# Optimization experiments

Measured on AMD Instinct MI355X. Metric: run time of the kernel, lower is better.

## Reference

```python
import jax, jax.numpy as jnp
import numpy as np

NEG_INF = -1e9


def setup_inputs() -> dict:
    key = jax.random.key(0)
    k1, k2, k3, k4 = jax.random.split(key, 4)
    B, H, M, N, D = 8, 16, 1024, 1024, 64
    return {
        "query": jax.random.normal(k1, (B, H, M, D), dtype=jnp.float32),
        "key": jax.random.normal(k2, (B, H, N, D), dtype=jnp.float32),
        "value": jax.random.normal(k3, (B, H, N, D), dtype=jnp.float32),
        "mask": jax.random.randint(k4, (B, H, N), 0, 2, dtype=jnp.int32),
    }


def reference(query, key, value, mask):
    # NOTE: faithful to source bug: scale uses key.size(-1) AFTER transpose,
    # i.e. N (sequence length), not d_h.
    N = key.shape[-2]
    scale = 1.0 / jnp.sqrt(jnp.asarray(N, dtype=query.dtype))
    # scores: [B, H, M, N]
    scores = jnp.einsum("bhmd,bhnd->bhmn", query, key) * scale
    scores = jnp.where(mask[:, :, None, :] == 0, jnp.asarray(NEG_INF, scores.dtype), scores)
    p_attn = jax.nn.softmax(scores, axis=-1)
    out = jnp.einsum("bhmn,bhnd->bhmd", p_attn, value)
    return out, p_attn
```

## Files before the change

kernel.cpp:

```cpp
#include <hip/hip_runtime.h>
#include <hip/hip_bf16.h>

#define BH 128
#define SEQ 1024
#define DH 64
#define MT 16
#define NW 256
#define PSTRIDE 1032

typedef __attribute__((ext_vector_type(8))) short short8;
typedef __attribute__((ext_vector_type(4))) float float4v;

__device__ __forceinline__ short bf16_rne(float x) {
    unsigned u = __builtin_bit_cast(unsigned, x);
    unsigned r = (u + 0x7fffu + ((u >> 16) & 1u)) >> 16;
    return (short)r;
}

__device__ __forceinline__ void bf16_split(float x, short& hi, short& lo) {
    unsigned u = __builtin_bit_cast(unsigned, x);
    hi = (short)(u >> 16);
    float hf = __builtin_bit_cast(float, u & 0xffff0000u);
    float res = x - hf;
    unsigned v = __builtin_bit_cast(unsigned, res);
    lo = (short)((v + 0x7fffu + ((v >> 16) & 1u)) >> 16);
}

__global__ __launch_bounds__(256, 4)
void attn_convert_kernel(const float* __restrict__ K, const float* __restrict__ V,
                         short* __restrict__ Khi, short* __restrict__ Klo,
                         short* __restrict__ Vt)
{
    const unsigned c = blockIdx.x * 256u + threadIdx.x;
    if (blockIdx.x < 4096) {
        const int bh = c >> 13;
        const int o8 = c & 8191;
        const int q  = o8 & 3;
        const int l  = (o8 >> 2) & 15;
        const int s  = (o8 >> 6) & 1;
        const int kb = o8 >> 7;
        const float* src = K + ((size_t)bh * SEQ + kb * 16 + l) * DH + s * 32 + q * 8;
        float4v x0 = *(const float4v*)src;
        float4v x1 = *(const float4v*)(src + 4);
        short8 hi, lo;
        #pragma unroll
        for (int j = 0; j < 4; ++j) {
            short h, w;
            bf16_split(x0[j], h, w); hi[j] = h;     lo[j] = w;
            bf16_split(x1[j], h, w); hi[4 + j] = h; lo[4 + j] = w;
        }
        *(short8*)(Khi + (size_t)c * 8) = hi;
        *(short8*)(Klo + (size_t)c * 8) = lo;
    } else {
        const unsigned c2 = c - 4096u * 256u;
        const int bh = c2 >> 13;
        const int o8 = c2 & 8191;
        const int lv = o8 & 15;
        const int k8 = (o8 >> 4) & 127;
        const int d4 = o8 >> 11;
        const float* src = V + ((size_t)bh * SEQ + k8 * 8) * DH + d4 * 16 + lv;
        short8 vv;
        #pragma unroll
        for (int j = 0; j < 8; ++j) vv[j] = bf16_rne(src[(size_t)j * DH]);
        *(short8*)(Vt + (size_t)c2 * 8) = vv;
    }
}

__global__ __launch_bounds__(256, 3)
void Attention_66889820668421_kernel(const float* __restrict__ Q,
                                     const short* __restrict__ Khi,
                                     const short* __restrict__ Klo,
                                     const short* __restrict__ Vt,
                                     const int*   __restrict__ mask,
                                     float* __restrict__ out,
                                     float* __restrict__ pattn)
{
    __shared__ short P_lds[MT * PSTRIDE];
    __shared__ float out_red[4][MT][DH];
    __shared__ float red_max[4][MT];
    __shared__ float red_sum[4][MT];

    const int tid  = threadIdx.x;
    const int wave = tid >> 6;
    const int lane = tid & 63;
    const int q    = lane >> 4;
    const int l    = lane & 15;
    const int bh   = blockIdx.y;
    const int m0   = blockIdx.x * MT;
    const int nbase = wave * NW;

    short8 a_hi[2], a_lo[2];
    {
        const float* qrow = Q + (size_t)(bh * SEQ + m0 + l) * DH;
        #pragma unroll
        for (int s = 0; s < 2; ++s) {
            float4v x0 = *(const float4v*)(qrow + s * 32 + q * 8);
            float4v x1 = *(const float4v*)(qrow + s * 32 + q * 8 + 4);
            #pragma unroll
            for (int j = 0; j < 4; ++j) {
                short h, lo2;
                bf16_split(x0[j], h, lo2); a_hi[s][j] = h; a_lo[s][j] = lo2;
                bf16_split(x1[j], h, lo2); a_hi[s][4 + j] = h; a_lo[s][4 + j] = lo2;
            }
        }
    }

    const short* khb = Khi + ((size_t)bh << 16);
    const short* klb = Klo + ((size_t)bh << 16);
    const short* vtb = Vt  + ((size_t)bh << 16);

    float4v acc[16];
    int mv[16];
    #pragma unroll
    for (int t = 0; t < 16; ++t) {
        const int kb   = (nbase >> 4) + t;
        const int off0 = kb * 1024 + l * 32 + q * 8;
        short8 b0h = *(const short8*)(khb + off0);
        short8 b0l = *(const short8*)(klb + off0);
        short8 b1h = *(const short8*)(khb + off0 + 512);
        short8 b1l = *(const short8*)(klb + off0 + 512);
        float4v a = {0.f, 0.f, 0.f, 0.f};
        a = __builtin_amdgcn_mfma_f32_16x16x32_bf16(a_hi[0], b0h, a, 0, 0, 0);
        a = __builtin_amdgcn_mfma_f32_16x16x32_bf16(a_hi[0], b0l, a, 0, 0, 0);
        a = __builtin_amdgcn_mfma_f32_16x16x32_bf16(a_lo[0], b0h, a, 0, 0, 0);
        a = __builtin_amdgcn_mfma_f32_16x16x32_bf16(a_hi[1], b1h, a, 0, 0, 0);
        a = __builtin_amdgcn_mfma_f32_16x16x32_bf16(a_hi[1], b1l, a, 0, 0, 0);
        a = __builtin_amdgcn_mfma_f32_16x16x32_bf16(a_lo[1], b1h, a, 0, 0, 0);
        mv[t] = mask[bh * SEQ + nbase + t * 16 + l];
        acc[t] = a;
    }

    const float scale = 0.03125f;
    float pm[4] = {-3e38f, -3e38f, -3e38f, -3e38f};
    #pragma unroll
    for (int t = 0; t < 16; ++t) {
        const bool ok = (mv[t] != 0);
        #pragma unroll
        for (int r = 0; r < 4; ++r) {
            float s = ok ? acc[t][r] * scale : -1e9f;
            acc[t][r] = s;
            pm[r] = fmaxf(pm[r], s);
        }
    }
    #pragma unroll
    for (int off = 1; off < 16; off <<= 1) {
        #pragma unroll
        for (int r = 0; r < 4; ++r)
            pm[r] = fmaxf(pm[r], __shfl_xor(pm[r], off));
    }
    if (l == 0) {
        #pragma unroll
        for (int r = 0; r < 4; ++r) red_max[wave][q * 4 + r] = pm[r];
    }
    __syncthreads();

    float rm[4];
    #pragma unroll
    for (int r = 0; r < 4; ++r) {
        const int row = q * 4 + r;
        rm[r] = fmaxf(fmaxf(red_max[0][row], red_max[1][row]),
                      fmaxf(red_max[2][row], red_max[3][row]));
    }

    float ps[4] = {0.f, 0.f, 0.f, 0.f};
    #pragma unroll
    for (int t = 0; t < 16; ++t) {
        #pragma unroll
        for (int r = 0; r < 4; ++r) {
            float e = __expf(acc[t][r] - rm[r]);
            acc[t][r] = e;
            ps[r] += e;
        }
    }
    #pragma unroll
    for (int off = 1; off < 16; off <<= 1) {
        #pragma unroll
        for (int r = 0; r < 4; ++r)
            ps[r] += __shfl_xor(ps[r], off);
    }
    if (l == 0) {
        #pragma unroll
        for (int r = 0; r < 4; ++r) red_sum[wave][q * 4 + r] = ps[r];
    }
    __syncthreads();

    float inv[4];
    #pragma unroll
    for (int r = 0; r < 4; ++r) {
        const int row = q * 4 + r;
        inv[r] = 1.0f / (red_sum[0][row] + red_sum[1][row] +
                         red_sum[2][row] + red_sum[3][row]);
    }

    float* prow = pattn + ((size_t)bh * SEQ + m0) * SEQ;
    #pragma unroll
    for (int t = 0; t < 16; ++t) {
        const int col = nbase + t * 16 + l;
        #pragma unroll
        for (int r = 0; r < 4; ++r) {
            const int row = q * 4 + r;
            float p = acc[t][r] * inv[r];
            __builtin_nontemporal_store(p, &prow[(size_t)row * SEQ + col]);
            P_lds[row * PSTRIDE + col] = bf16_rne(p);
        }
    }
    __syncthreads();

    float4v ao[4];
    #pragma unroll
    for (int dt = 0; dt < 4; ++dt) ao[dt] = (float4v){0.f, 0.f, 0.f, 0.f};

    #pragma unroll
    for (int step = 0; step < 8; ++step) {
        const int key0 = nbase + step * 32;
        short8 pa = *(const short8*)&P_lds[l * PSTRIDE + key0 + q * 8];
        const int k8q = (key0 >> 3) + q;
        #pragma unroll
        for (int dt = 0; dt < 4; ++dt) {
            short8 vb = *(const short8*)(vtb + ((size_t)(dt * 128 + k8q) * 16 + l) * 8);
            ao[dt] = __builtin_amdgcn_mfma_f32_16x16x32_bf16(pa, vb, ao[dt], 0, 0, 0);
        }
    }

    #pragma unroll
    for (int dt = 0; dt < 4; ++dt) {
        #pragma unroll
        for (int r = 0; r < 4; ++r)
            out_red[wave][q * 4 + r][dt * 16 + l] = ao[dt][r];
    }
    __syncthreads();

    #pragma unroll
    for (int i = 0; i < 4; ++i) {
        const int e = tid + 256 * i;
        const int row = e >> 6;
        const int d = e & 63;
        float s = out_red[0][row][d] + out_red[1][row][d] +
                  out_red[2][row][d] + out_red[3][row][d];
        __builtin_nontemporal_store(s, &out[(size_t)(bh * SEQ + m0 + row) * DH + d]);
    }
}

__global__ __launch_bounds__(256, 2)
void Attention_66889820668421_fallback(const float* __restrict__ Q,
                                       const float* __restrict__ K,
                                       const float* __restrict__ V,
                                       const int*   __restrict__ mask,
                                       float* __restrict__ out,
                                       float* __restrict__ pattn)
{
    __shared__ short P_lds[MT * PSTRIDE];
    __shared__ float out_red[4][MT][DH];
    __shared__ float red_max[4][MT];
    __shared__ float red_sum[4][MT];

    const int tid  = threadIdx.x;
    const int wave = tid >> 6;
    const int lane = tid & 63;
    const int q    = lane >> 4;
    const int l    = lane & 15;
    const int bh   = blockIdx.y;
    const int m0   = blockIdx.x * MT;
    const int nbase = wave * NW;

    short8 a_hi[2], a_lo[2];
    {
        const float* qrow = Q + (size_t)(bh * SEQ + m0 + l) * DH;
        #pragma unroll
        for (int s = 0; s < 2; ++s) {
            float4v x0 = *(const float4v*)(qrow + s * 32 + q * 8);
            float4v x1 = *(const float4v*)(qrow + s * 32 + q * 8 + 4);
            #pragma unroll
            for (int j = 0; j < 4; ++j) {
                short h, lo2;
                bf16_split(x0[j], h, lo2); a_hi[s][j] = h; a_lo[s][j] = lo2;
                bf16_split(x1[j], h, lo2); a_hi[s][4 + j] = h; a_lo[s][4 + j] = lo2;
            }
        }
    }

    float4v acc[16];
    int mv[16];
    #pragma unroll
    for (int t = 0; t < 16; ++t) {
        const int key = nbase + t * 16 + l;
        const float* krow = K + (size_t)(bh * SEQ + key) * DH;
        float4v a = {0.f, 0.f, 0.f, 0.f};
        #pragma unroll
        for (int s = 0; s < 2; ++s) {
            float4v x0 = *(const float4v*)(krow + s * 32 + q * 8);
            float4v x1 = *(const float4v*)(krow + s * 32 + q * 8 + 4);
            short8 bhh, bll;
            #pragma unroll
            for (int j = 0; j < 4; ++j) {
                short h, lo2;
                bf16_split(x0[j], h, lo2); bhh[j] = h; bll[j] = lo2;
                bf16_split(x1[j], h, lo2); bhh[4 + j] = h; bll[4 + j] = lo2;
            }
            a = __builtin_amdgcn_mfma_f32_16x16x32_bf16(a_hi[s], bhh, a, 0, 0, 0);
            a = __builtin_amdgcn_mfma_f32_16x16x32_bf16(a_hi[s], bll, a, 0, 0, 0);
            a = __builtin_amdgcn_mfma_f32_16x16x32_bf16(a_lo[s], bhh, a, 0, 0, 0);
        }
        mv[t] = mask[bh * SEQ + nbase + t * 16 + l];
        acc[t] = a;
    }

    const float scale = 0.03125f;
    float pm[4] = {-3e38f, -3e38f, -3e38f, -3e38f};
    #pragma unroll
    for (int t = 0; t < 16; ++t) {
        const bool ok = (mv[t] != 0);
        #pragma unroll
        for (int r = 0; r < 4; ++r) {
            float s = ok ? acc[t][r] * scale : -1e9f;
            acc[t][r] = s;
            pm[r] = fmaxf(pm[r], s);
        }
    }
    #pragma unroll
    for (int off = 1; off < 16; off <<= 1) {
        #pragma unroll
        for (int r = 0; r < 4; ++r)
            pm[r] = fmaxf(pm[r], __shfl_xor(pm[r], off));
    }
    if (l == 0) {
        #pragma unroll
        for (int r = 0; r < 4; ++r) red_max[wave][q * 4 + r] = pm[r];
    }
    __syncthreads();

    float rm[4];
    #pragma unroll
    for (int r = 0; r < 4; ++r) {
        const int row = q * 4 + r;
        rm[r] = fmaxf(fmaxf(red_max[0][row], red_max[1][row]),
                      fmaxf(red_max[2][row], red_max[3][row]));
    }

    float ps[4] = {0.f, 0.f, 0.f, 0.f};
    #pragma unroll
    for (int t = 0; t < 16; ++t) {
        #pragma unroll
        for (int r = 0; r < 4; ++r) {
            float e = __expf(acc[t][r] - rm[r]);
            acc[t][r] = e;
            ps[r] += e;
        }
    }
    #pragma unroll
    for (int off = 1; off < 16; off <<= 1) {
        #pragma unroll
        for (int r = 0; r < 4; ++r)
            ps[r] += __shfl_xor(ps[r], off);
    }
    if (l == 0) {
        #pragma unroll
        for (int r = 0; r < 4; ++r) red_sum[wave][q * 4 + r] = ps[r];
    }
    __syncthreads();

    float inv[4];
    #pragma unroll
    for (int r = 0; r < 4; ++r) {
        const int row = q * 4 + r;
        inv[r] = 1.0f / (red_sum[0][row] + red_sum[1][row] +
                         red_sum[2][row] + red_sum[3][row]);
    }

    float* prow = pattn + ((size_t)bh * SEQ + m0) * SEQ;
    #pragma unroll
    for (int t = 0; t < 16; ++t) {
        const int col = nbase + t * 16 + l;
        #pragma unroll
        for (int r = 0; r < 4; ++r) {
            const int row = q * 4 + r;
            float p = acc[t][r] * inv[r];
            prow[(size_t)row * SEQ + col] = p;
            P_lds[row * PSTRIDE + col] = bf16_rne(p);
        }
    }
    __syncthreads();

    float4v ao[4];
    #pragma unroll
    for (int dt = 0; dt < 4; ++dt) ao[dt] = (float4v){0.f, 0.f, 0.f, 0.f};

    #pragma unroll 2
    for (int step = 0; step < 8; ++step) {
        const int key0 = nbase + step * 32;
        short8 pa = *(const short8*)&P_lds[l * PSTRIDE + key0 + q * 8];
        const float* vbase = V + (size_t)(bh * SEQ + key0 + q * 8) * DH + l;
        #pragma unroll
        for (int dt = 0; dt < 4; ++dt) {
            short8 vb;
            #pragma unroll
            for (int j = 0; j < 8; ++j)
                vb[j] = bf16_rne(vbase[(size_t)j * DH + dt * 16]);
            ao[dt] = __builtin_amdgcn_mfma_f32_16x16x32_bf16(pa, vb, ao[dt], 0, 0, 0);
        }
    }

    #pragma unroll
    for (int dt = 0; dt < 4; ++dt) {
        #pragma unroll
        for (int r = 0; r < 4; ++r)
            out_red[wave][q * 4 + r][dt * 16 + l] = ao[dt][r];
    }
    __syncthreads();

    #pragma unroll
    for (int i = 0; i < 4; ++i) {
        const int e = tid + 256 * i;
        const int row = e >> 6;
        const int d = e & 63;
        float s = out_red[0][row][d] + out_red[1][row][d] +
                  out_red[2][row][d] + out_red[3][row][d];
        out[(size_t)(bh * SEQ + m0 + row) * DH + d] = s;
    }
}

extern "C" void kernel_launch(void* const* d_in, const int* in_sizes, int n_in,
                              void* d_out, int out_size, void* d_ws, size_t ws_size,
                              hipStream_t stream) {
    const float* Q    = (const float*)d_in[0];
    const float* K    = (const float*)d_in[1];
    const float* V    = (const float*)d_in[2];
    const int*   mask = (const int*)d_in[3];
    float* out   = (float*)d_out;
    float* pattn = out + (size_t)BH * SEQ * DH;

    const size_t elems = (size_t)BH * SEQ * DH;
    const size_t need  = elems * sizeof(short) * 3;

    dim3 grid(SEQ / MT, BH);
    if (ws_size >= need) {
        short* Khi = (short*)d_ws;
        short* Klo = Khi + elems;
        short* Vt  = Klo + elems;
        attn_convert_kernel<<<dim3(8192), 256, 0, stream>>>(K, V, Khi, Klo, Vt);
        Attention_66889820668421_kernel<<<grid, 256, 0, stream>>>(Q, Khi, Klo, Vt,
                                                                  mask, out, pattn);
    } else {
        Attention_66889820668421_fallback<<<grid, 256, 0, stream>>>(Q, K, V, mask,
                                                                    out, pattn);
    }
}
```

Baseline: 788.6 us.

## Split PV matmul across waves by output dim instead of key range

Each wave now computes a 16-column slice of the output over all keys, instead of a partial sum over its own key range for all 64 columns. This removes the out_red shared buffer, the extra barrier and the cross-wave reduction, and it frees LDS so launch bounds can be raised to 4 blocks per CU. In exchange each wave reads P rows written by other waves (already synced) and does a longer serial MFMA chain on a single accumulator.

```diff
diff --git a/kernel.cpp b/kernel.cpp
--- a/kernel.cpp
+++ b/kernel.cpp
@@ -66,7 +66,7 @@
     }
 }
 
-__global__ __launch_bounds__(256, 3)
+__global__ __launch_bounds__(256, 4)
 void Attention_66889820668421_kernel(const float* __restrict__ Q,
                                      const short* __restrict__ Khi,
                                      const short* __restrict__ Klo,
@@ -76,7 +76,6 @@
                                      float* __restrict__ pattn)
 {
     __shared__ short P_lds[MT * PSTRIDE];
-    __shared__ float out_red[4][MT][DH];
     __shared__ float red_max[4][MT];
     __shared__ float red_sum[4][MT];
 
@@ -206,38 +205,21 @@
     }
     __syncthreads();
 
-    float4v ao[4];
-    #pragma unroll
-    for (int dt = 0; dt < 4; ++dt) ao[dt] = (float4v){0.f, 0.f, 0.f, 0.f};
-
-    #pragma unroll
-    for (int step = 0; step < 8; ++step) {
-        const int key0 = nbase + step * 32;
+    float4v ao = {0.f, 0.f, 0.f, 0.f};
+    const short* vwb = vtb + (size_t)wave * 16384;
+    #pragma unroll 4
+    for (int step = 0; step < 32; ++step) {
+        const int key0 = step * 32;
         short8 pa = *(const short8*)&P_lds[l * PSTRIDE + key0 + q * 8];
-        const int k8q = (key0 >> 3) + q;
-        #pragma unroll
-        for (int dt = 0; dt < 4; ++dt) {
-            short8 vb = *(const short8*)(vtb + ((size_t)(dt * 128 + k8q) * 16 + l) * 8);
-            ao[dt] = __builtin_amdgcn_mfma_f32_16x16x32_bf16(pa, vb, ao[dt], 0, 0, 0);
-        }
-    }
-
-    #pragma unroll
-    for (int dt = 0; dt < 4; ++dt) {
-        #pragma unroll
-        for (int r = 0; r < 4; ++r)
-            out_red[wave][q * 4 + r][dt * 16 + l] = ao[dt][r];
-    }
-    __syncthreads();
-
-    #pragma unroll
-    for (int i = 0; i < 4; ++i) {
-        const int e = tid + 256 * i;
-        const int row = e >> 6;
-        const int d = e & 63;
-        float s = out_red[0][row][d] + out_red[1][row][d] +
-                  out_red[2][row][d] + out_red[3][row][d];
-        __builtin_nontemporal_store(s, &out[(size_t)(bh * SEQ + m0 + row) * DH + d]);
+        short8 vb = *(const short8*)(vwb + (((size_t)((key0 >> 3) + q)) * 16 + l) * 8);
+        ao = __builtin_amdgcn_mfma_f32_16x16x32_bf16(pa, vb, ao, 0, 0, 0);
+    }
+
+    const int d = wave * 16 + l;
+    #pragma unroll
+    for (int r = 0; r < 4; ++r) {
+        const int row = q * 4 + r;
+        __builtin_nontemporal_store(ao[r], &out[(size_t)(bh * SEQ + m0 + row) * DH + d]);
     }
 }
 
```

After: 782.1 us. No clear change (-0.8%).
